# Kernel tuning notes

Hardware: AMD Instinct MI355X
Metric: run time of the kernel (lower is better)

The kernel has to match this reference:

```python
import jax, jax.numpy as jnp
import numpy as np

EPS = 1e-5  # torch BatchNorm1d default eps


def _bn(x, gamma, beta):
    # training-mode BatchNorm1d over the point dimension
    m = jnp.mean(x, axis=0)
    v = jnp.var(x, axis=0)
    return (x - m) * jax.lax.rsqrt(v + EPS) * gamma + beta


def setup_inputs() -> dict:
    key = jax.random.key(0)
    ks = jax.random.split(key, 8)
    N, D = 1000000, 9
    G, V = 32, 32768  # 32^3 voxel grid; with 1M points all voxels occupied w.h.p.
    feats = jax.random.normal(ks[0], (N, D), dtype=jnp.float32)
    coords = jax.random.randint(ks[1], (N, 3), 0, G, dtype=jnp.int32)

    def lin(k, fan_in, fan_out):
        kw, kb = jax.random.split(k)
        s = 1.0 / np.sqrt(fan_in)
        W = jax.random.uniform(kw, (fan_in, fan_out), jnp.float32, -s, s)
        b = jax.random.uniform(kb, (fan_out,), jnp.float32, -s, s)
        return W, b

    W1, b1 = lin(ks[2], 9, 64)
    W2, b2 = lin(ks[3], 64, 128)
    W3, b3 = lin(ks[4], 128, 256)
    W4, b4 = lin(ks[5], 256, 256)
    return {
        'feats': feats, 'coords': coords, 'num_voxels': V,
        'g0': jnp.ones((9,), jnp.float32), 'be0': jnp.zeros((9,), jnp.float32),
        'W1': W1, 'b1': b1,
        'g1': jnp.ones((64,), jnp.float32), 'be1': jnp.zeros((64,), jnp.float32),
        'W2': W2, 'b2': b2,
        'g2': jnp.ones((128,), jnp.float32), 'be2': jnp.zeros((128,), jnp.float32),
        'W3': W3, 'b3': b3,
        'g3': jnp.ones((256,), jnp.float32), 'be3': jnp.zeros((256,), jnp.float32),
        'W4': W4, 'b4': b4,
    }


def _mlp(x, g0, be0, W1, b1, g1, be1, W2, b2, g2, be2, W3, b3, g3, be3, W4, b4):
    x = _bn(x, g0, be0)
    x = jax.nn.relu(_bn(x @ W1 + b1, g1, be1))
    x = jax.nn.relu(_bn(x @ W2 + b2, g2, be2))
    x = jax.nn.relu(_bn(x @ W3 + b3, g3, be3))
    return x @ W4 + b4


def reference(feats, coords, num_voxels, g0, be0, W1, b1, g1, be1, W2, b2,
              g2, be2, W3, b3, g3, be3, W4, b4):
    # NOTE: the torch module shuffles points first; unique(dim=0) is sorted and
    # scatter_max is permutation-invariant, so the shuffle does not affect output.
    unq_coords, unq_inv = jnp.unique(
        coords, axis=0, return_inverse=True, size=num_voxels, fill_value=0)
    unq_inv = unq_inv.reshape(-1)
    unq_coords = unq_coords.astype(jnp.int64)
    h = _mlp(feats, g0, be0, W1, b1, g1, be1, W2, b2, g2, be2, W3, b3, g3, be3, W4, b4)
    pooled = jax.ops.segment_max(h, unq_inv, num_segments=num_voxels)  # [V, 256]
    return pooled, unq_coords
```

## Files before the change

kernel.cpp:

```cpp
#include <hip/hip_runtime.h>
#include <math.h>

#define TPB 256
#define NVOX 32768
#define BN_EPS 1e-5f

typedef short s16x8 __attribute__((ext_vector_type(8)));
typedef short s16x4 __attribute__((ext_vector_type(4)));
typedef float f32x4 __attribute__((ext_vector_type(4)));

#define P0_OFF     0u
#define P1_OFF     256u
#define P2_OFF     (P1_OFF + 64u*128u*4u)
#define P3_OFF     (P2_OFF + 64u*256u*4u)
#define PAR_END    (P3_OFF + 64u*512u*4u)
#define A0_OFF     229632u
#define C0_OFF     229888u
#define A1_OFF     230144u
#define C1_OFF     230400u
#define A2_OFF     230656u
#define C2_OFF     231680u
#define A3_OFF     232704u
#define C3_OFF     233728u
#define HIST_OFF   234752u
#define BASE_OFF   (HIST_OFF + 131072u)
#define CURS_OFF   (BASE_OFF + 131328u)
#define WT1_OFF    (CURS_OFF + 131072u)
#define WT2_OFF    (WT1_OFF + 4096u)
#define WT3_OFF    (WT2_OFF + 16384u)
#define WT4_OFF    (WT3_OFF + 65536u)
#define X_OFF      4845568u

__device__ __forceinline__ unsigned short f2bf(float f) {
    unsigned u = __float_as_uint(f);
    u += 0x7FFFu + ((u >> 16) & 1u);
    return (unsigned short)(u >> 16);
}
__device__ __forceinline__ unsigned short f2bft(float f) {
    return (unsigned short)(__float_as_uint(f) >> 16);
}
__device__ __forceinline__ float bf2f(unsigned short h) {
    return __uint_as_float(((unsigned)h) << 16);
}

template<int ROWB>
__device__ __forceinline__ int swz(int row, int b) {
    constexpr int M = (ROWB >= 128) ? 7 : ((ROWB >= 64) ? 3 : 1);
    return row * ROWB + (b ^ ((row & M) << 4));
}

__device__ __forceinline__ s16x4 bn_relu_pack(f32x4 acc, f32x4 av, f32x4 cv) {
    s16x4 pk;
#pragma unroll
    for (int r = 0; r < 4; ++r) pk[r] = (short)f2bft(fmaxf(fmaf(acc[r], av[r], cv[r]), 0.f));
    return pk;
}

template<int NOUT>
__device__ __forceinline__ void stats_red(f32x4 ps, f32x4 pq, int ch, float* prow) {
#pragma unroll
    for (int m = 1; m <= 8; m <<= 1) {
#pragma unroll
        for (int r = 0; r < 4; ++r) { ps[r] += __shfl_xor(ps[r], m); pq[r] += __shfl_xor(pq[r], m); }
    }
    if ((threadIdx.x & 15) == 0) {
#pragma unroll
        for (int r = 0; r < 4; ++r) {
            atomicAdd(&prow[ch + r], ps[r]);
            atomicAdd(&prow[NOUT + ch + r], pq[r]);
        }
    }
}

__global__ void k_prepw(const float* __restrict__ W1, const float* __restrict__ W2,
                        const float* __restrict__ W3, const float* __restrict__ W4,
                        unsigned short* __restrict__ wt1, unsigned short* __restrict__ wt2,
                        unsigned short* __restrict__ wt3, unsigned short* __restrict__ wt4) {
    for (int i = blockIdx.x * blockDim.x + threadIdx.x; i < 108544;
         i += gridDim.x * blockDim.x) {
        if (i < 2048) {
            int n = i >> 5, k = i & 31;
            wt1[i] = (k < 9) ? f2bf(W1[k * 64 + n]) : (unsigned short)0;
        } else if (i < 10240) {
            int j = i - 2048; int n = j >> 6, k = j & 63;
            wt2[j] = f2bf(W2[k * 128 + n]);
        } else if (i < 43008) {
            int j = i - 10240; int n = j >> 7, k = j & 127;
            wt3[j] = f2bf(W3[k * 256 + n]);
        } else {
            int j = i - 43008; int n = j >> 8, k = j & 255;
            wt4[j] = f2bf(W4[k * 256 + n]);
        }
    }
}

__global__ void k_hist_stats(const int* __restrict__ coords, const float* __restrict__ feats,
                             int N, unsigned* __restrict__ hist, float* __restrict__ banks) {
    float S[9] = {0}, G[45] = {0};
    for (int i = blockIdx.x * blockDim.x + threadIdx.x; i < N;
         i += gridDim.x * blockDim.x) {
        int v = (coords[3 * i] << 10) | (coords[3 * i + 1] << 5) | coords[3 * i + 2];
        atomicAdd(&hist[v], 1u);
        const float* r = feats + (size_t)i * 9;
        float x[9];
#pragma unroll
        for (int c = 0; c < 9; ++c) { x[c] = r[c]; S[c] += x[c]; }
        int idx = 0;
#pragma unroll
        for (int c = 0; c < 9; ++c)
#pragma unroll
            for (int c2 = 0; c2 <= c; ++c2) { G[idx] = fmaf(x[c], x[c2], G[idx]); ++idx; }
    }
#pragma unroll
    for (int m = 1; m <= 32; m <<= 1) {
#pragma unroll
        for (int c = 0; c < 9; ++c) S[c] += __shfl_xor(S[c], m);
#pragma unroll
        for (int j = 0; j < 45; ++j) G[j] += __shfl_xor(G[j], m);
    }
    if ((threadIdx.x & 63) == 0) {
        float* b = banks + (size_t)(blockIdx.x & 63) * 54;
#pragma unroll
        for (int c = 0; c < 9; ++c) atomicAdd(&b[c], S[c]);
#pragma unroll
        for (int j = 0; j < 45; ++j) atomicAdd(&b[9 + j], G[j]);
    }
}

__global__ void k_fin0(const float* __restrict__ banks, float* __restrict__ SG,
                       const float* __restrict__ g0, const float* __restrict__ be0,
                       float* __restrict__ A0, float* __restrict__ C0, float n) {
    __shared__ float sg[54];
    const int t = threadIdx.x;
    if (t < 54) {
        float s = 0.f;
        for (int b = 0; b < 64; ++b) s += banks[b * 54 + t];
        sg[t] = s; SG[t] = s;
    }
    __syncthreads();
    if (t < 9) {
        float m = sg[t] / n;
        float v = sg[9 + t * (t + 1) / 2 + t] / n - m * m;
        float a = g0[t] * rsqrtf(v + BN_EPS);
        A0[t] = a; C0[t] = be0[t] - m * a;
    }
}

__global__ void k_fin1(const float* __restrict__ SG,
                       const float* __restrict__ A0, const float* __restrict__ C0,
                       const float* __restrict__ W1, const float* __restrict__ b1,
                       const float* __restrict__ g1, const float* __restrict__ be1,
                       float* __restrict__ A1, float* __restrict__ C1, float n) {
    __shared__ float Sz[9], Gz[81];
    const int t = threadIdx.x;
    if (t < 9) Sz[t] = A0[t] * SG[t] + n * C0[t];
    if (t < 81) {
        const int c = t / 9, c2 = t - 9 * (t / 9);
        const int i = c > c2 ? c : c2, j = c > c2 ? c2 : c;
        const float G = SG[9 + i * (i + 1) / 2 + j];
        Gz[t] = A0[c] * A0[c2] * G + A0[c] * SG[c] * C0[c2]
              + C0[c] * A0[c2] * SG[c2] + n * C0[c] * C0[c2];
    }
    __syncthreads();
    if (t < 64) {
        float wn[9];
#pragma unroll
        for (int c = 0; c < 9; ++c) wn[c] = W1[c * 64 + t];
        float su = 0.f, qq = 0.f;
#pragma unroll
        for (int c = 0; c < 9; ++c) {
            su = fmaf(wn[c], Sz[c], su);
#pragma unroll
            for (int c2 = 0; c2 < 9; ++c2) qq = fmaf(wn[c] * wn[c2], Gz[c * 9 + c2], qq);
        }
        const float bb = b1[t];
        const float mean = (su + n * bb) / n;
        const float q = qq + 2.f * bb * su + n * bb * bb;
        const float var = q / n - mean * mean;
        const float a = g1[t] * rsqrtf(var + BN_EPS);
        A1[t] = a;
        C1[t] = fmaf(a, bb, be1[t] - mean * a);
    }
}

__global__ void k_scan(const unsigned* __restrict__ hist, int* __restrict__ base,
                       unsigned* __restrict__ cursor, int N) {
    __shared__ unsigned part[1024];
    const int t = threadIdx.x;
    unsigned sum = 0;
    for (int j = 0; j < 32; ++j) sum += hist[t * 32 + j];
    part[t] = sum;
    __syncthreads();
    for (int d = 1; d < 1024; d <<= 1) {
        unsigned v = (t >= d) ? part[t - d] : 0u;
        __syncthreads();
        part[t] += v;
        __syncthreads();
    }
    unsigned run = part[t] - sum;
    for (int j = 0; j < 32; ++j) {
        unsigned h = hist[t * 32 + j];
        base[t * 32 + j] = (int)run;
        cursor[t * 32 + j] = run;
        run += h;
    }
    if (t == 1023) base[32768] = (int)run;
}

__global__ void k_scatter2(const int* __restrict__ coords, const float* __restrict__ feats,
                           int N, unsigned* __restrict__ cursor,
                           const float* __restrict__ A0, const float* __restrict__ C0,
                           unsigned short* __restrict__ Xg) {
    float a0[9], c0[9];
#pragma unroll
    for (int c = 0; c < 9; ++c) { a0[c] = A0[c]; c0[c] = C0[c]; }
    for (int i = blockIdx.x * blockDim.x + threadIdx.x; i < N;
         i += gridDim.x * blockDim.x) {
        int v = (coords[3 * i] << 10) | (coords[3 * i + 1] << 5) | coords[3 * i + 2];
        unsigned pos = atomicAdd(&cursor[v], 1u);
        const float* r = feats + (size_t)i * 9;
        s16x8 lo, hi;
#pragma unroll
        for (int c = 0; c < 8; ++c) lo[c] = (short)f2bf(fmaf(r[c], a0[c], c0[c]));
        hi = (s16x8){0, 0, 0, 0, 0, 0, 0, 0};
        hi[0] = (short)f2bf(fmaf(r[8], a0[8], c0[8]));
        *(s16x8*)(Xg + (size_t)pos * 16) = lo;
        *(s16x8*)(Xg + (size_t)pos * 16 + 8) = hi;
    }
}

__global__ void k_fin(const float* __restrict__ part, int nparts, int C,
                      const float* __restrict__ g, const float* __restrict__ be,
                      const float* __restrict__ bias,
                      float* __restrict__ A, float* __restrict__ Cc, float n) {
    int c = threadIdx.x;
    if (c >= C) return;
    float s = 0.f, q = 0.f;
    for (int r = 0; r < nparts; ++r) { s += part[r * 2 * C + c]; q += part[r * 2 * C + C + c]; }
    float m = s / n;
    float v = q / n - m * m;
    float a = g[c] * rsqrtf(v + BN_EPS);
    float cc = be[c] - m * a;
    A[c] = a;
    Cc[c] = bias ? fmaf(a, bias[c], cc) : cc;
}

__global__ void k_coords(float* __restrict__ outc) {
    int v = blockIdx.x * blockDim.x + threadIdx.x;
    if (v < NVOX) {
        outc[3 * v + 0] = (float)(v >> 10);
        outc[3 * v + 1] = (float)((v >> 5) & 31);
        outc[3 * v + 2] = (float)(v & 31);
    }
}

__global__ __launch_bounds__(256) void k_pass2(
    const unsigned short* __restrict__ Xg,
    const unsigned short* __restrict__ wt1, const unsigned short* __restrict__ wt2,
    const float* __restrict__ A1, const float* __restrict__ C1,
    const float* __restrict__ b2,
    float* __restrict__ p2, int N, int nt) {
    __shared__ char act1[2][16384];
    const int tid = threadIdx.x;
    const int w = tid >> 6, lane = tid & 63, g = lane >> 4, lq = lane & 15;
    const int chb1 = w * 16, chb2 = w * 32;
    const int mask = (lq & 7) << 4;
    char* const a1w  = act1[0] + lq * 128 + (((chb1 + g * 4) * 2) ^ mask);
    char* const a1r0 = act1[0] + lq * 128 + ((g * 16) ^ mask);
    char* const a1r1 = act1[0] + lq * 128 + ((64 + g * 16) ^ mask);

    const s16x8 a1 = *(const s16x8*)(wt1 + (chb1 + lq) * 32 + g * 8);
    s16x8 w2f[2][2];
#pragma unroll
    for (int mt = 0; mt < 2; ++mt)
#pragma unroll
        for (int kc = 0; kc < 2; ++kc)
            w2f[mt][kc] = *(const s16x8*)(wt2 + (size_t)(chb2 + mt * 16 + lq) * 64 + kc * 32 + g * 8);
    const int ch1 = chb1 + g * 4;
    const f32x4 av1 = *(const f32x4*)(A1 + ch1);
    const f32x4 cv1 = *(const f32x4*)(C1 + ch1);
    f32x4 bv2[2];
#pragma unroll
    for (int mt = 0; mt < 2; ++mt) bv2[mt] = *(const f32x4*)(b2 + chb2 + mt * 16 + g * 4);
    f32x4 ps[2], pq[2];
#pragma unroll
    for (int mt = 0; mt < 2; ++mt) { ps[mt] = (f32x4){0.f,0.f,0.f,0.f}; pq[mt] = (f32x4){0.f,0.f,0.f,0.f}; }

    int t = blockIdx.x;
    if (t < nt) {
#pragma unroll
        for (int ct = 0; ct < 8; ++ct) {
            const s16x8 b = *(const s16x8*)(Xg + (size_t)(t * 128 + ct * 16 + lq) * 16 + g * 8);
            f32x4 a = (f32x4){0.f,0.f,0.f,0.f};
            a = __builtin_amdgcn_mfma_f32_16x16x32_bf16(a1, b, a, 0, 0, 0);
            *(s16x4*)(a1w + ct * 2048) = bn_relu_pack(a, av1, cv1);
        }
        __syncthreads();
        int cur = 0;
        while (true) {
            const int tn = t + gridDim.x;
            const bool more = tn < nt;
            const int t0 = t * 128;
            const int co = cur << 14;
            f32x4 acc2[2][8];
#pragma unroll
            for (int mt = 0; mt < 2; ++mt)
#pragma unroll
                for (int ct = 0; ct < 8; ++ct) acc2[mt][ct] = (f32x4){0.f,0.f,0.f,0.f};
#pragma unroll
            for (int kc = 0; kc < 2; ++kc) {
                char* const rb = (kc ? a1r1 : a1r0) + co;
#pragma unroll
                for (int ct = 0; ct < 8; ++ct) {
                    const s16x8 b = *(const s16x8*)(rb + ct * 2048);
#pragma unroll
                    for (int mt = 0; mt < 2; ++mt)
                        acc2[mt][ct] = __builtin_amdgcn_mfma_f32_16x16x32_bf16(w2f[mt][kc], b, acc2[mt][ct], 0, 0, 0);
                }
            }
#pragma unroll
            for (int mt = 0; mt < 2; ++mt)
#pragma unroll
                for (int ct = 0; ct < 8; ++ct) {
                    const bool valid = (t0 + ct * 16 + lq) < N;
#pragma unroll
                    for (int r = 0; r < 4; ++r) {
                        const float h = valid ? (acc2[mt][ct][r] + bv2[mt][r]) : 0.f;
                        ps[mt][r] += h; pq[mt][r] += h * h;
                    }
                }
            if (more) {
                char* const wb = a1w + (co ^ 16384);
#pragma unroll
                for (int ct = 0; ct < 8; ++ct) {
                    const s16x8 b = *(const s16x8*)(Xg + (size_t)(tn * 128 + ct * 16 + lq) * 16 + g * 8);
                    f32x4 a = (f32x4){0.f,0.f,0.f,0.f};
                    a = __builtin_amdgcn_mfma_f32_16x16x32_bf16(a1, b, a, 0, 0, 0);
                    *(s16x4*)(wb + ct * 2048) = bn_relu_pack(a, av1, cv1);
                }
            }
            __syncthreads();
            if (!more) break;
            t = tn; cur ^= 1;
        }
    }
    float* prow = p2 + (blockIdx.x & 63) * 256;
#pragma unroll
    for (int mt = 0; mt < 2; ++mt)
        stats_red<128>(ps[mt], pq[mt], chb2 + mt * 16 + g * 4, prow);
}

__global__ __launch_bounds__(512) void k_pass3(
    const unsigned short* __restrict__ Xg,
    const unsigned short* __restrict__ wt1, const unsigned short* __restrict__ wt2,
    const unsigned short* __restrict__ wt3,
    const float* __restrict__ A1, const float* __restrict__ C1,
    const float* __restrict__ A2, const float* __restrict__ C2,
    const float* __restrict__ b3,
    float* __restrict__ p3, int N, int nt) {
    __shared__ char act1[8192];
    __shared__ char act2[16384];
    const int tid = threadIdx.x;
    const int w = tid >> 6, lane = tid & 63, g = lane >> 4, lq = lane & 15;
    const int wm = w >> 1, wn = w & 1;
    const int chb1 = wm * 16, chb2 = w * 16, chb3 = w * 32;
    const int mask = (lq & 7) << 4;
    char* const a1w  = act1 + (wn * 32 + lq) * 128 + (((chb1 + g * 4) * 2) ^ mask);
    char* const a1r0 = act1 + lq * 128 + ((g * 16) ^ mask);
    char* const a1r1 = act1 + lq * 128 + ((64 + g * 16) ^ mask);
    char* const a2w  = act2 + lq * 256 + (((chb2 + g * 4) * 2) ^ mask);
    char* const a2r0 = act2 + lq * 256 + ((g * 16) ^ mask);
    char* const a2r1 = act2 + lq * 256 + ((64 + g * 16) ^ mask);

    const s16x8 a1 = *(const s16x8*)(wt1 + (chb1 + lq) * 32 + g * 8);
    s16x8 w2f[2], w3f[2][4];
#pragma unroll
    for (int kc = 0; kc < 2; ++kc)
        w2f[kc] = *(const s16x8*)(wt2 + (size_t)(chb2 + lq) * 64 + kc * 32 + g * 8);
#pragma unroll
    for (int mt = 0; mt < 2; ++mt)
#pragma unroll
        for (int kc = 0; kc < 4; ++kc)
            w3f[mt][kc] = *(const s16x8*)(wt3 + (size_t)(chb3 + mt * 16 + lq) * 128 + kc * 32 + g * 8);
    const int ch1 = chb1 + g * 4, ch2 = chb2 + g * 4;
    const f32x4 av1 = *(const f32x4*)(A1 + ch1);
    const f32x4 cv1 = *(const f32x4*)(C1 + ch1);
    const f32x4 av2 = *(const f32x4*)(A2 + ch2);
    const f32x4 cv2 = *(const f32x4*)(C2 + ch2);
    f32x4 bv3[2];
#pragma unroll
    for (int mt = 0; mt < 2; ++mt) bv3[mt] = *(const f32x4*)(b3 + chb3 + mt * 16 + g * 4);
    f32x4 ps[2], pq[2];
#pragma unroll
    for (int mt = 0; mt < 2; ++mt) { ps[mt] = (f32x4){0.f,0.f,0.f,0.f}; pq[mt] = (f32x4){0.f,0.f,0.f,0.f}; }

    int t = blockIdx.x;
    if (t < nt) {
#pragma unroll
        for (int ct = 0; ct < 2; ++ct) {
            const int row = wn * 32 + ct * 16 + lq;
            const s16x8 b = *(const s16x8*)(Xg + (size_t)(t * 64 + row) * 16 + g * 8);
            f32x4 a = (f32x4){0.f,0.f,0.f,0.f};
            a = __builtin_amdgcn_mfma_f32_16x16x32_bf16(a1, b, a, 0, 0, 0);
            *(s16x4*)(a1w + ct * 2048) = bn_relu_pack(a, av1, cv1);
        }
        __syncthreads();
        {
            f32x4 acc[4];
#pragma unroll
            for (int ct = 0; ct < 4; ++ct) acc[ct] = (f32x4){0.f,0.f,0.f,0.f};
#pragma unroll
            for (int kc = 0; kc < 2; ++kc) {
                char* const rb = kc ? a1r1 : a1r0;
#pragma unroll
                for (int ct = 0; ct < 4; ++ct) {
                    const s16x8 b = *(const s16x8*)(rb + ct * 2048);
                    acc[ct] = __builtin_amdgcn_mfma_f32_16x16x32_bf16(w2f[kc], b, acc[ct], 0, 0, 0);
                }
            }
#pragma unroll
            for (int ct = 0; ct < 4; ++ct)
                *(s16x4*)(a2w + ct * 4096) = bn_relu_pack(acc[ct], av2, cv2);
        }
        __syncthreads();
        while (true) {
            const int tn = t + gridDim.x;
            const bool more = tn < nt;
            s16x8 xb[2];
            if (more) {
#pragma unroll
                for (int ct = 0; ct < 2; ++ct) {
                    const int row = wn * 32 + ct * 16 + lq;
                    xb[ct] = *(const s16x8*)(Xg + (size_t)(tn * 64 + row) * 16 + g * 8);
                }
            }
            {
                f32x4 acc[2][4];
#pragma unroll
                for (int mt = 0; mt < 2; ++mt)
#pragma unroll
                    for (int ct = 0; ct < 4; ++ct) acc[mt][ct] = (f32x4){0.f,0.f,0.f,0.f};
#pragma unroll
                for (int kc = 0; kc < 4; ++kc) {
                    char* const rb = ((kc & 1) ? a2r1 : a2r0) + (kc >> 1) * 128;
#pragma unroll
                    for (int ct = 0; ct < 4; ++ct) {
                        const s16x8 b = *(const s16x8*)(rb + ct * 4096);
#pragma unroll
                        for (int mt = 0; mt < 2; ++mt)
                            acc[mt][ct] = __builtin_amdgcn_mfma_f32_16x16x32_bf16(w3f[mt][kc], b, acc[mt][ct], 0, 0, 0);
                    }
                }
                const int t0 = t * 64;
#pragma unroll
                for (int mt = 0; mt < 2; ++mt)
#pragma unroll
                    for (int ct = 0; ct < 4; ++ct) {
                        const bool valid = (t0 + ct * 16 + lq) < N;
#pragma unroll
                        for (int r = 0; r < 4; ++r) {
                            const float h = valid ? (acc[mt][ct][r] + bv3[mt][r]) : 0.f;
                            ps[mt][r] += h; pq[mt][r] += h * h;
                        }
                    }
            }
            if (more) {
#pragma unroll
                for (int ct = 0; ct < 2; ++ct) {
                    f32x4 a = (f32x4){0.f,0.f,0.f,0.f};
                    a = __builtin_amdgcn_mfma_f32_16x16x32_bf16(a1, xb[ct], a, 0, 0, 0);
                    *(s16x4*)(a1w + ct * 2048) = bn_relu_pack(a, av1, cv1);
                }
            }
            __syncthreads();
            if (more) {
                f32x4 acc[4];
#pragma unroll
                for (int ct = 0; ct < 4; ++ct) acc[ct] = (f32x4){0.f,0.f,0.f,0.f};
#pragma unroll
                for (int kc = 0; kc < 2; ++kc) {
                    char* const rb = kc ? a1r1 : a1r0;
#pragma unroll
                    for (int ct = 0; ct < 4; ++ct) {
                        const s16x8 b = *(const s16x8*)(rb + ct * 2048);
                        acc[ct] = __builtin_amdgcn_mfma_f32_16x16x32_bf16(w2f[kc], b, acc[ct], 0, 0, 0);
                    }
                }
#pragma unroll
                for (int ct = 0; ct < 4; ++ct)
                    *(s16x4*)(a2w + ct * 4096) = bn_relu_pack(acc[ct], av2, cv2);
            }
            __syncthreads();
            if (!more) break;
            t = tn;
        }
    }
    float* prow = p3 + (blockIdx.x & 63) * 512;
#pragma unroll
    for (int mt = 0; mt < 2; ++mt)
        stats_red<256>(ps[mt], pq[mt], chb3 + mt * 16 + g * 4, prow);
}

__global__ __launch_bounds__(1024, 4) void k_pass4(
    const unsigned short* __restrict__ Xg,
    const unsigned short* __restrict__ wt1, const unsigned short* __restrict__ wt2,
    const unsigned short* __restrict__ wt3, const unsigned short* __restrict__ wt4,
    const float* __restrict__ A1, const float* __restrict__ C1,
    const float* __restrict__ A2, const float* __restrict__ C2,
    const float* __restrict__ A3, const float* __restrict__ C3,
    const float* __restrict__ b4,
    const int* __restrict__ base, float* __restrict__ out) {
    extern __shared__ char smem[];
    char* act1 = smem;
    char* act2 = smem + 8192;
    char* act3 = smem + 24576;
    char* h4   = smem + 57344;

    const int tid = threadIdx.x;
    const int w = tid >> 6, lane = tid & 63, g = lane >> 4, lq = lane & 15;
    const int c1 = (w & 3) * 16, p1 = (w >> 2) * 16;
    const int c2 = (w & 7) * 16, p2 = (w >> 3) * 32;
    const int c3 = w * 16;
    const int mask = (lq & 7) << 4;
    char* const a1w  = act1 + (p1 + lq) * 128 + (((c1 + g * 4) * 2) ^ mask);
    char* const a1r0 = act1 + (p2 + lq) * 128 + ((g * 16) ^ mask);
    char* const a1r1 = act1 + (p2 + lq) * 128 + ((64 + g * 16) ^ mask);
    char* const a2w  = act2 + (p2 + lq) * 256 + (((c2 + g * 4) * 2) ^ mask);
    char* const a2r0 = act2 + lq * 256 + ((g * 16) ^ mask);
    char* const a2r1 = act2 + lq * 256 + ((64 + g * 16) ^ mask);
    char* const a3w  = act3 + lq * 512 + (((c3 + g * 4) * 2) ^ mask);
    char* const a3r0 = act3 + lq * 512 + ((g * 16) ^ mask);
    char* const a3r1 = act3 + lq * 512 + ((64 + g * 16) ^ mask);
    char* const h4w  = h4 + lq * 512 + (((c3 + g * 4) * 2) ^ mask);

    const int vb = blockIdx.x * 32;
    const int pstart = base[vb], pend = base[vb + 32];
    const int chgrp = tid & 31, slot = tid >> 5;
    const int vlo = base[vb + slot], vhi = base[vb + slot + 1];

    const s16x8 a1 = *(const s16x8*)(wt1 + (c1 + lq) * 32 + g * 8);
    s16x8 w2f[2], w3f[4], w4f[8];
#pragma unroll
    for (int kc = 0; kc < 2; ++kc)
        w2f[kc] = *(const s16x8*)(wt2 + (size_t)(c2 + lq) * 64 + kc * 32 + g * 8);
#pragma unroll
    for (int kc = 0; kc < 4; ++kc)
        w3f[kc] = *(const s16x8*)(wt3 + (size_t)(c3 + lq) * 128 + kc * 32 + g * 8);
#pragma unroll
    for (int kc = 0; kc < 8; ++kc)
        w4f[kc] = *(const s16x8*)(wt4 + (size_t)(c3 + lq) * 256 + kc * 32 + g * 8);

    const f32x4 av1 = *(const f32x4*)(A1 + c1 + g * 4);
    const f32x4 cv1 = *(const f32x4*)(C1 + c1 + g * 4);
    const f32x4 av2 = *(const f32x4*)(A2 + c2 + g * 4);
    const f32x4 cv2 = *(const f32x4*)(C2 + c2 + g * 4);
    const f32x4 av3 = *(const f32x4*)(A3 + c3 + g * 4);
    const f32x4 cv3 = *(const f32x4*)(C3 + c3 + g * 4);
    const f32x4 bv4 = *(const f32x4*)(b4 + c3 + g * 4);

    float rmax[8];
#pragma unroll
    for (int j = 0; j < 8; ++j) rmax[j] = -INFINITY;

    if (pstart < pend) {
        {
            const s16x8 b = *(const s16x8*)(Xg + (size_t)(pstart + p1 + lq) * 16 + g * 8);
            f32x4 a = (f32x4){0.f,0.f,0.f,0.f};
            a = __builtin_amdgcn_mfma_f32_16x16x32_bf16(a1, b, a, 0, 0, 0);
            *(s16x4*)a1w = bn_relu_pack(a, av1, cv1);
        }
        __syncthreads();
        {
            f32x4 acc[2];
#pragma unroll
            for (int ct = 0; ct < 2; ++ct) acc[ct] = (f32x4){0.f,0.f,0.f,0.f};
#pragma unroll
            for (int kc = 0; kc < 2; ++kc) {
                char* const rb = kc ? a1r1 : a1r0;
#pragma unroll
                for (int ct = 0; ct < 2; ++ct) {
                    const s16x8 b = *(const s16x8*)(rb + ct * 2048);
                    acc[ct] = __builtin_amdgcn_mfma_f32_16x16x32_bf16(w2f[kc], b, acc[ct], 0, 0, 0);
                }
            }
#pragma unroll
            for (int ct = 0; ct < 2; ++ct)
                *(s16x4*)(a2w + ct * 4096) = bn_relu_pack(acc[ct], av2, cv2);
        }
        __syncthreads();

        int lt = pstart;
        for (int t0 = pstart; t0 < pend; t0 += 64) {
            const int nxt = t0 + 64;
            const bool more = nxt < pend;
            s16x8 xb;
            if (more)
                xb = *(const s16x8*)(Xg + (size_t)(nxt + p1 + lq) * 16 + g * 8);
            {
                f32x4 acc[4];
#pragma unroll
                for (int ct = 0; ct < 4; ++ct) acc[ct] = (f32x4){0.f,0.f,0.f,0.f};
#pragma unroll
                for (int kc = 0; kc < 4; ++kc) {
                    char* const rb = ((kc & 1) ? a2r1 : a2r0) + (kc >> 1) * 128;
#pragma unroll
                    for (int ct = 0; ct < 4; ++ct) {
                        const s16x8 b = *(const s16x8*)(rb + ct * 4096);
                        acc[ct] = __builtin_amdgcn_mfma_f32_16x16x32_bf16(w3f[kc], b, acc[ct], 0, 0, 0);
                    }
                }
#pragma unroll
                for (int ct = 0; ct < 4; ++ct)
                    *(s16x4*)(a3w + ct * 8192) = bn_relu_pack(acc[ct], av3, cv3);
            }
            if (t0 > pstart) {
                const int tm = t0 - 64;
                const int lo = max(vlo, tm), hi = min(vhi, tm + 64);
                for (int p = lo; p < hi; ++p) {
                    const int row = p - tm;
                    const s16x8 hv = *(const s16x8*)(h4 + row * 512 + ((chgrp * 16) ^ ((row & 7) << 4)));
#pragma unroll
                    for (int j = 0; j < 8; ++j)
                        rmax[j] = fmaxf(rmax[j], bf2f((unsigned short)hv[j]));
                }
            }
            if (more) {
                f32x4 a = (f32x4){0.f,0.f,0.f,0.f};
                a = __builtin_amdgcn_mfma_f32_16x16x32_bf16(a1, xb, a, 0, 0, 0);
                *(s16x4*)a1w = bn_relu_pack(a, av1, cv1);
            }
            __syncthreads();
            if (more) {
                f32x4 acc[2];
#pragma unroll
                for (int ct = 0; ct < 2; ++ct) acc[ct] = (f32x4){0.f,0.f,0.f,0.f};
#pragma unroll
                for (int kc = 0; kc < 2; ++kc) {
                    char* const rb = kc ? a1r1 : a1r0;
#pragma unroll
                    for (int ct = 0; ct < 2; ++ct) {
                        const s16x8 b = *(const s16x8*)(rb + ct * 2048);
                        acc[ct] = __builtin_amdgcn_mfma_f32_16x16x32_bf16(w2f[kc], b, acc[ct], 0, 0, 0);
                    }
                }
#pragma unroll
                for (int ct = 0; ct < 2; ++ct)
                    *(s16x4*)(a2w + ct * 4096) = bn_relu_pack(acc[ct], av2, cv2);
            }
            {
                f32x4 acc[4];
#pragma unroll
                for (int ct = 0; ct < 4; ++ct) acc[ct] = (f32x4){0.f,0.f,0.f,0.f};
#pragma unroll
                for (int kc = 0; kc < 8; ++kc) {
                    char* const rb = ((kc & 1) ? a3r1 : a3r0) + (kc >> 1) * 128;
#pragma unroll
                    for (int ct = 0; ct < 4; ++ct) {
                        const s16x8 b = *(const s16x8*)(rb + ct * 8192);
                        acc[ct] = __builtin_amdgcn_mfma_f32_16x16x32_bf16(w4f[kc], b, acc[ct], 0, 0, 0);
                    }
                }
#pragma unroll
                for (int ct = 0; ct < 4; ++ct) {
                    s16x4 pk;
#pragma unroll
                    for (int r = 0; r < 4; ++r) pk[r] = (short)f2bf(acc[ct][r] + bv4[r]);
                    *(s16x4*)(h4w + ct * 8192) = pk;
                }
            }
            __syncthreads();
            lt = t0;
        }
        {
            const int lo = max(vlo, lt), hi = min(vhi, lt + 64);
            for (int p = lo; p < hi; ++p) {
                const int row = p - lt;
                const s16x8 hv = *(const s16x8*)(h4 + row * 512 + ((chgrp * 16) ^ ((row & 7) << 4)));
#pragma unroll
                for (int j = 0; j < 8; ++j)
                    rmax[j] = fmaxf(rmax[j], bf2f((unsigned short)hv[j]));
            }
        }
    }
    float* orow = out + (size_t)(vb + slot) * 256 + chgrp * 8;
    f32x4 o0, o1;
#pragma unroll
    for (int j = 0; j < 4; ++j) { o0[j] = rmax[j]; o1[j] = rmax[4 + j]; }
    *(f32x4*)orow = o0;
    *(f32x4*)(orow + 4) = o1;
}

extern "C" void kernel_launch(void* const* d_in, const int* in_sizes, int n_in,
                              void* d_out, int out_size, void* d_ws, size_t ws_size,
                              hipStream_t stream) {
    const float* feats = (const float*)d_in[0];
    const int* coords = (const int*)d_in[1];
    const float* g0 = (const float*)d_in[3];
    const float* be0 = (const float*)d_in[4];
    const float* W1 = (const float*)d_in[5];
    const float* b1 = (const float*)d_in[6];
    const float* g1 = (const float*)d_in[7];
    const float* be1 = (const float*)d_in[8];
    const float* W2 = (const float*)d_in[9];
    const float* b2 = (const float*)d_in[10];
    const float* g2 = (const float*)d_in[11];
    const float* be2 = (const float*)d_in[12];
    const float* W3 = (const float*)d_in[13];
    const float* b3 = (const float*)d_in[14];
    const float* g3 = (const float*)d_in[15];
    const float* be3 = (const float*)d_in[16];
    const float* W4 = (const float*)d_in[17];
    const float* b4 = (const float*)d_in[18];
    float* out = (float*)d_out;
    char* ws = (char*)d_ws;

    const int N = in_sizes[0] / 9;
    const float fN = (float)N;
    const int nt128 = (N + 127) / 128;
    const int nt64 = (N + 63) / 64;

    unsigned short* Xg = (unsigned short*)(ws + X_OFF);
    const unsigned short* wt1 = (const unsigned short*)(ws + WT1_OFF);
    const unsigned short* wt2 = (const unsigned short*)(ws + WT2_OFF);
    const unsigned short* wt3 = (const unsigned short*)(ws + WT3_OFF);
    const unsigned short* wt4 = (const unsigned short*)(ws + WT4_OFF);
    float* A0 = (float*)(ws + A0_OFF); float* C0 = (float*)(ws + C0_OFF);
    float* A1 = (float*)(ws + A1_OFF); float* C1 = (float*)(ws + C1_OFF);
    float* A2 = (float*)(ws + A2_OFF); float* C2 = (float*)(ws + C2_OFF);
    float* A3 = (float*)(ws + A3_OFF); float* C3 = (float*)(ws + C3_OFF);

    hipMemsetAsync(ws, 0, PAR_END, stream);
    hipMemsetAsync(ws + HIST_OFF, 0, 131072, stream);
    {
        const size_t rows = (size_t)nt128 * 128;
        hipMemsetAsync(ws + X_OFF + (size_t)N * 32u, 0,
                       (rows - (size_t)N) * 32u + 8192u, stream);
    }

    hipFuncSetAttribute((const void*)k_pass4,
        hipFuncAttributeMaxDynamicSharedMemorySize, 90112);

    k_prepw<<<128, TPB, 0, stream>>>(W1, W2, W3, W4,
        (unsigned short*)(ws + WT1_OFF), (unsigned short*)(ws + WT2_OFF),
        (unsigned short*)(ws + WT3_OFF), (unsigned short*)(ws + WT4_OFF));
    k_hist_stats<<<1024, TPB, 0, stream>>>(coords, feats, N,
        (unsigned*)(ws + HIST_OFF), (float*)(ws + P1_OFF));
    k_fin0<<<1, 64, 0, stream>>>((const float*)(ws + P1_OFF), (float*)(ws + P0_OFF),
                                 g0, be0, A0, C0, fN);
    k_fin1<<<1, 128, 0, stream>>>((const float*)(ws + P0_OFF), A0, C0,
                                  W1, b1, g1, be1, A1, C1, fN);
    k_scan<<<1, 1024, 0, stream>>>((const unsigned*)(ws + HIST_OFF),
                                   (int*)(ws + BASE_OFF), (unsigned*)(ws + CURS_OFF), N);
    k_scatter2<<<1024, TPB, 0, stream>>>(coords, feats, N, (unsigned*)(ws + CURS_OFF),
                                         A0, C0, Xg);
    k_coords<<<(NVOX + TPB - 1) / TPB, TPB, 0, stream>>>(out + (size_t)NVOX * 256);

    k_pass2<<<2048, 256, 0, stream>>>(Xg, wt1, wt2, A1, C1, b2,
                                      (float*)(ws + P2_OFF), N, nt128);
    k_fin<<<1, TPB, 0, stream>>>((const float*)(ws + P2_OFF), 64, 128, g2, be2, b2,
                                 A2, C2, fN);

    k_pass3<<<2048, 512, 0, stream>>>(Xg, wt1, wt2, wt3, A1, C1, A2, C2, b3,
                                      (float*)(ws + P3_OFF), N, nt64);
    k_fin<<<1, TPB, 0, stream>>>((const float*)(ws + P3_OFF), 64, 256, g3, be3, b3,
                                 A3, C3, fN);

    k_pass4<<<NVOX / 32, 1024, 90112, stream>>>(Xg, wt1, wt2, wt3, wt4,
        A1, C1, A2, C2, A3, C3, b4, (const int*)(ws + BASE_OFF), out);
}
```

Measured before the change: 932.3 us.

## Split layer-4 GEMM over K halves with 2x32 output tiles per wave

Layer 4 was computed with each of 16 waves owning 16 output channels over the full K=256. Now each wave owns 32 output channels and half of K, so each B fragment loaded from LDS feeds two MFMAs, halving act3 reads. The two K-half partial sums are combined through LDS: kh=1 waves store bf16 partials, a barrier follows, and kh=0 waves add them with the bias. This costs an extra __syncthreads, extra LDS traffic, and an intermediate bf16 rounding of the partial sum, which slightly changes numerics.

```diff
diff --git a/kernel.cpp b/kernel.cpp
--- a/kernel.cpp
+++ b/kernel.cpp
@@ -521,6 +521,7 @@
     const int c1 = (w & 3) * 16, p1 = (w >> 2) * 16;
     const int c2 = (w & 7) * 16, p2 = (w >> 3) * 32;
     const int c3 = w * 16;
+    const int c4 = (w & 7) * 32, kh = w >> 3;
     const int mask = (lq & 7) << 4;
     char* const a1w  = act1 + (p1 + lq) * 128 + (((c1 + g * 4) * 2) ^ mask);
     char* const a1r0 = act1 + (p2 + lq) * 128 + ((g * 16) ^ mask);
@@ -529,9 +530,10 @@
     char* const a2r0 = act2 + lq * 256 + ((g * 16) ^ mask);
     char* const a2r1 = act2 + lq * 256 + ((64 + g * 16) ^ mask);
     char* const a3w  = act3 + lq * 512 + (((c3 + g * 4) * 2) ^ mask);
-    char* const a3r0 = act3 + lq * 512 + ((g * 16) ^ mask);
-    char* const a3r1 = act3 + lq * 512 + ((64 + g * 16) ^ mask);
-    char* const h4w  = h4 + lq * 512 + (((c3 + g * 4) * 2) ^ mask);
+    char* const a3r0 = act3 + lq * 512 + ((kh * 256 + g * 16) ^ mask);
+    char* const a3r1 = act3 + lq * 512 + ((kh * 256 + 64 + g * 16) ^ mask);
+    char* const h4w0 = h4 + lq * 512 + (((c4 + g * 4) * 2) ^ mask);
+    char* const h4w1 = h4 + lq * 512 + (((c4 + 16 + g * 4) * 2) ^ mask);
 
     const int vb = blockIdx.x * 32;
     const int pstart = base[vb], pend = base[vb + 32];
@@ -539,7 +541,7 @@
     const int vlo = base[vb + slot], vhi = base[vb + slot + 1];
 
     const s16x8 a1 = *(const s16x8*)(wt1 + (c1 + lq) * 32 + g * 8);
-    s16x8 w2f[2], w3f[4], w4f[8];
+    s16x8 w2f[2], w3f[4], w4f[2][4];
 #pragma unroll
     for (int kc = 0; kc < 2; ++kc)
         w2f[kc] = *(const s16x8*)(wt2 + (size_t)(c2 + lq) * 64 + kc * 32 + g * 8);
@@ -547,8 +549,10 @@
     for (int kc = 0; kc < 4; ++kc)
         w3f[kc] = *(const s16x8*)(wt3 + (size_t)(c3 + lq) * 128 + kc * 32 + g * 8);
 #pragma unroll
-    for (int kc = 0; kc < 8; ++kc)
-        w4f[kc] = *(const s16x8*)(wt4 + (size_t)(c3 + lq) * 256 + kc * 32 + g * 8);
+    for (int mt = 0; mt < 2; ++mt)
+#pragma unroll
+        for (int kc = 0; kc < 4; ++kc)
+            w4f[mt][kc] = *(const s16x8*)(wt4 + (size_t)(c4 + mt * 16 + lq) * 256 + kh * 128 + kc * 32 + g * 8);
 
     const f32x4 av1 = *(const f32x4*)(A1 + c1 + g * 4);
     const f32x4 cv1 = *(const f32x4*)(C1 + c1 + g * 4);
@@ -556,7 +560,9 @@
     const f32x4 cv2 = *(const f32x4*)(C2 + c2 + g * 4);
     const f32x4 av3 = *(const f32x4*)(A3 + c3 + g * 4);
     const f32x4 cv3 = *(const f32x4*)(C3 + c3 + g * 4);
-    const f32x4 bv4 = *(const f32x4*)(b4 + c3 + g * 4);
+    f32x4 bv4[2];
+#pragma unroll
+    for (int mt = 0; mt < 2; ++mt) bv4[mt] = *(const f32x4*)(b4 + c4 + mt * 16 + g * 4);
 
     float rmax[8];
 #pragma unroll
@@ -630,6 +636,11 @@
                 *(s16x4*)a1w = bn_relu_pack(a, av1, cv1);
             }
             __syncthreads();
+            f32x4 acc4[2][4];
+#pragma unroll
+            for (int mt = 0; mt < 2; ++mt)
+#pragma unroll
+                for (int ct = 0; ct < 4; ++ct) acc4[mt][ct] = (f32x4){0.f,0.f,0.f,0.f};
             if (more) {
                 f32x4 acc[2];
 #pragma unroll
@@ -647,25 +658,44 @@
                 for (int ct = 0; ct < 2; ++ct)
                     *(s16x4*)(a2w + ct * 4096) = bn_relu_pack(acc[ct], av2, cv2);
             }
-            {
-                f32x4 acc[4];
-#pragma unroll
-                for (int ct = 0; ct < 4; ++ct) acc[ct] = (f32x4){0.f,0.f,0.f,0.f};
-#pragma unroll
-                for (int kc = 0; kc < 8; ++kc) {
-                    char* const rb = ((kc & 1) ? a3r1 : a3r0) + (kc >> 1) * 128;
+#pragma unroll
+            for (int kc = 0; kc < 4; ++kc) {
+                char* const rb = ((kc & 1) ? a3r1 : a3r0) + (kc >> 1) * 128;
+#pragma unroll
+                for (int ct = 0; ct < 4; ++ct) {
+                    const s16x8 b = *(const s16x8*)(rb + ct * 8192);
+#pragma unroll
+                    for (int mt = 0; mt < 2; ++mt)
+                        acc4[mt][ct] = __builtin_amdgcn_mfma_f32_16x16x32_bf16(w4f[mt][kc], b, acc4[mt][ct], 0, 0, 0);
+                }
+            }
+            if (kh == 1) {
+#pragma unroll
+                for (int mt = 0; mt < 2; ++mt) {
+                    char* const hw = mt ? h4w1 : h4w0;
 #pragma unroll
                     for (int ct = 0; ct < 4; ++ct) {
-                        const s16x8 b = *(const s16x8*)(rb + ct * 8192);
-                        acc[ct] = __builtin_amdgcn_mfma_f32_16x16x32_bf16(w4f[kc], b, acc[ct], 0, 0, 0);
+                        s16x4 pk;
+#pragma unroll
+                        for (int r = 0; r < 4; ++r) pk[r] = (short)f2bf(acc4[mt][ct][r]);
+                        *(s16x4*)(hw + ct * 8192) = pk;
                     }
                 }
-#pragma unroll
-                for (int ct = 0; ct < 4; ++ct) {
-                    s16x4 pk;
-#pragma unroll
-                    for (int r = 0; r < 4; ++r) pk[r] = (short)f2bf(acc[ct][r] + bv4[r]);
-                    *(s16x4*)(h4w + ct * 8192) = pk;
+            }
+            __syncthreads();
+            if (kh == 0) {
+#pragma unroll
+                for (int mt = 0; mt < 2; ++mt) {
+                    char* const hw = mt ? h4w1 : h4w0;
+#pragma unroll
+                    for (int ct = 0; ct < 4; ++ct) {
+                        const s16x4 pv = *(const s16x4*)(hw + ct * 8192);
+                        s16x4 pk;
+#pragma unroll
+                        for (int r = 0; r < 4; ++r)
+                            pk[r] = (short)f2bf(acc4[mt][ct][r] + bf2f((unsigned short)pv[r]) + bv4[mt][r]);
+                        *(s16x4*)(hw + ct * 8192) = pk;
+                    }
                 }
             }
             __syncthreads();
```

After: 1.167 ms. 25.2% more time.
